# Performance work log

Hardware: AMD Instinct MI355X
Metric: run time of the kernel (lower is better)

The kernel has to match this reference:

```python
import jax, jax.numpy as jnp
import numpy as np

B, C, D, H = 2, 512, 512, 8
DH = D // H  # d_head = 64


def setup_inputs() -> dict:
    key = jax.random.key(0)
    ks = jax.random.split(key, 8)
    init = lambda k, shape: 0.02 * jax.random.normal(k, shape, dtype=jnp.float32)
    return {
        "x": jax.random.normal(ks[0], (B, C, D), dtype=jnp.float32),
        "Wq": init(ks[1], (D, D)), "bq": jnp.zeros((D,), jnp.float32),
        "Wk": init(ks[2], (D, D)), "bk": jnp.zeros((D,), jnp.float32),
        "Wv": init(ks[3], (D, D)), "bv": jnp.zeros((D,), jnp.float32),
        "W1": init(ks[4], (3 * DH, DH)), "b1": jnp.zeros((DH,), jnp.float32),
        "W2": init(ks[5], (DH, 1)), "b2": jnp.zeros((1,), jnp.float32),
        "Wo": init(ks[6], (D, D)), "bo": jnp.zeros((D,), jnp.float32),
    }


def reference(x, Wq, bq, Wk, bk, Wv, bv, W1, b1, W2, b2, Wo, bo):
    b, c, dm = x.shape
    # projections -> [B, H, C, d_head]
    q = (x @ Wq + bq).reshape(b, c, H, DH).transpose(0, 2, 1, 3)
    k = (x @ Wk + bk).reshape(b, c, H, DH).transpose(0, 2, 1, 3)
    v = (x @ Wv + bv).reshape(b, c, H, DH).transpose(0, 2, 1, 3)
    # split first MLP weight: [q || k || q*k] @ W1 = q@W1q + k@W1k + (q*k)@W1i
    W1q, W1k, W1i = W1[:DH], W1[DH:2 * DH], W1[2 * DH:]
    hq = jnp.einsum('bhid,de->bhie', q, W1q)   # [B,H,C,d]
    hk = jnp.einsum('bhjd,de->bhje', k, W1k)   # [B,H,C,d]
    hi = jnp.einsum('bhid,bhjd,de->bhije', q, k, W1i)  # [B,H,C,C,d] dominant intermediate
    h = hi + hq[:, :, :, None, :] + hk[:, :, None, :, :] + b1
    g = jax.nn.gelu(h, approximate=False)  # torch nn.GELU is exact erf form
    scores = (jnp.einsum('bhije,e->bhij', g, W2[:, 0]) + b2[0]) / (DH ** 0.5)
    attn = jax.nn.softmax(scores, axis=-1)  # dropout is identity in eval
    out = jnp.einsum('bhij,bhjd->bhid', attn, v)
    out = out.transpose(0, 2, 1, 3).reshape(b, c, dm)
    return out @ Wo + bo
```

## Files before the change

### kernel.cpp

```cpp
#include <hip/hip_runtime.h>
#include <hip/hip_bf16.h>
#include <math.h>

#define BB 2
#define CC 512
#define DD 512
#define HH 8
#define DH 64
#define TI 8

typedef __attribute__((ext_vector_type(8))) short short8;
typedef __attribute__((ext_vector_type(16))) float floatx16;
typedef __attribute__((ext_vector_type(2))) float float2v;
typedef unsigned short u16;

__device__ __forceinline__ float fast_rcp(float x) {
#if __has_builtin(__builtin_amdgcn_rcpf)
    return __builtin_amdgcn_rcpf(x);
#else
    return 1.0f / x;
#endif
}

__device__ __forceinline__ unsigned f2bf(float f) {
    unsigned u = __float_as_uint(f);
    u += 0x7FFF + ((u >> 16) & 1);
    return u >> 16;
}

__device__ __forceinline__ unsigned pk_bf16(float a, float b) {
    __hip_bfloat162 h2 = __float22bfloat162_rn(make_float2(a, b));
    unsigned r;
    __builtin_memcpy(&r, &h2, 4);
    return r;
}

__device__ __forceinline__ short8 mk_short8(unsigned u0, unsigned u1,
                                            unsigned u2, unsigned u3) {
    uint4 u = make_uint4(u0, u1, u2, u3);
    short8 r;
    __builtin_memcpy(&r, &u, 16);
    return r;
}

__device__ __forceinline__ float2v pkfma(float2v a, float2v b, float2v c) {
#if __has_builtin(__builtin_elementwise_fma)
    return __builtin_elementwise_fma(a, b, c);
#else
    float2v r; r[0] = fmaf(a[0], b[0], c[0]); r[1] = fmaf(a[1], b[1], c[1]);
    return r;
#endif
}

__device__ __forceinline__ void split_pack(const float* src, unsigned* hpk, unsigned* lpk) {
    #pragma unroll
    for (int p = 0; p < 4; ++p) {
        float a = src[2 * p], b = src[2 * p + 1];
        unsigned hp = pk_bf16(a, b);
        float la = a - __uint_as_float(hp << 16);
        float lb = b - __uint_as_float(hp & 0xffff0000u);
        hpk[p] = hp;
        lpk[p] = pk_bf16(la, lb);
    }
}

#define GC0 0.3989422804f
#define GC1 (-0.0664903801f)

__device__ __forceinline__ float2v gelu_dot2(float2v h, float2v w2, float2v p) {
    float2v s = h * h;
    float2v q = pkfma(s, float2v{GC1, GC1}, float2v{GC0, GC0});
    float2v t = s * q;
    float2v g = pkfma(h, float2v{0.5f, 0.5f}, t);
    return pkfma(g, w2, p);
}

__global__ __launch_bounds__(256) void prep(
    const float* __restrict__ Wq, const float* __restrict__ Wk,
    const float* __restrict__ Wv, const float* __restrict__ Wo,
    const float* __restrict__ W1, const float* __restrict__ b1,
    const float* __restrict__ bq,
    u16* __restrict__ wth, u16* __restrict__ wtl,
    u16* __restrict__ woh, u16* __restrict__ wol,
    float* __restrict__ b1p)
{
    __shared__ float SH[3 * 64 * 68];
    int j = blockIdx.x, t = threadIdx.x;
    if (j < 256) {
        int mat = j >> 6;
        const float* W = (mat == 0) ? Wq : (mat == 1) ? Wk : (mat == 2) ? Wv : Wo;
        u16* oh = (mat < 3) ? wth + (size_t)mat * 262144 : woh;
        u16* ol = (mat < 3) ? wtl + (size_t)mat * 262144 : wol;
        int tile = j & 63;
        int k0 = (tile >> 3) * 64, n0 = (tile & 7) * 64;
        float (*TT)[68] = (float(*)[68])SH;
        int r = t >> 4, c4 = (t & 15) * 4;
        #pragma unroll
        for (int rr = 0; rr < 4; ++rr) {
            int k = r + rr * 16;
            float4 v = *(const float4*)&W[(size_t)(k0 + k) * 512 + n0 + c4];
            TT[c4 + 0][k] = v.x; TT[c4 + 1][k] = v.y;
            TT[c4 + 2][k] = v.z; TT[c4 + 3][k] = v.w;
        }
        __syncthreads();
        int n = t >> 2, kc = (t & 3) * 16;
        #pragma unroll
        for (int g = 0; g < 2; ++g) {
            unsigned hpk[4], lpk[4];
            split_pack(&TT[n][kc + g * 8], hpk, lpk);
            *(uint4*)&oh[(size_t)(n0 + n) * 512 + k0 + kc + g * 8] =
                make_uint4(hpk[0], hpk[1], hpk[2], hpk[3]);
            *(uint4*)&ol[(size_t)(n0 + n) * 512 + k0 + kc + g * 8] =
                make_uint4(lpk[0], lpk[1], lpk[2], lpk[3]);
        }
    } else if (j < 320) {
        int jj = j - 256;
        int D0 = (jj >> 3) * 64, h = jj & 7;
        float (*WQ)[68]  = (float(*)[68])SH;
        float (*W1Q)[68] = (float(*)[68])(SH + 64 * 68);
        float (*OT)[68]  = (float(*)[68])(SH + 2 * 64 * 68);
        int r = t >> 4, c4 = (t & 15) * 4;
        #pragma unroll
        for (int rr = 0; rr < 4; ++rr) {
            int d = r + rr * 16;
            *(float4*)&WQ[d][c4]  = *(const float4*)&Wq[(size_t)(D0 + d) * 512 + h * 64 + c4];
            *(float4*)&W1Q[d][c4] = *(const float4*)&W1[(size_t)d * 64 + c4];
        }
        __syncthreads();
        int D = t & 63, ec = (t >> 6) * 16;
        float outv[16];
        #pragma unroll
        for (int i = 0; i < 16; ++i) outv[i] = 0.0f;
        for (int d4 = 0; d4 < 16; ++d4) {
            float4 wq4 = *(float4*)&WQ[D][d4 * 4];
            float wqa[4] = {wq4.x, wq4.y, wq4.z, wq4.w};
            #pragma unroll
            for (int dd = 0; dd < 4; ++dd) {
                float wv_ = wqa[dd];
                const float* wrow = &W1Q[d4 * 4 + dd][ec];
                #pragma unroll
                for (int i = 0; i < 16; ++i) outv[i] = fmaf(wv_, wrow[i], outv[i]);
            }
        }
        #pragma unroll
        for (int i = 0; i < 16; ++i) OT[ec + i][D] = outv[i];
        __syncthreads();
        int n = t >> 2, kc = (t & 3) * 16;
        u16* oh3 = wth + (size_t)3 * 262144;
        u16* ol3 = wtl + (size_t)3 * 262144;
        #pragma unroll
        for (int g = 0; g < 2; ++g) {
            unsigned hpk[4], lpk[4];
            split_pack(&OT[n][kc + g * 8], hpk, lpk);
            *(uint4*)&oh3[(size_t)(h * 64 + n) * 512 + D0 + kc + g * 8] =
                make_uint4(hpk[0], hpk[1], hpk[2], hpk[3]);
            *(uint4*)&ol3[(size_t)(h * 64 + n) * 512 + D0 + kc + g * 8] =
                make_uint4(lpk[0], lpk[1], lpk[2], lpk[3]);
        }
    } else {
        for (int n = t; n < 512; n += 256) {
            int h = n >> 6, e = n & 63;
            float s = b1[e];
            for (int d = 0; d < 64; ++d)
                s = fmaf(bq[h * 64 + d], W1[(size_t)d * 64 + e], s);
            b1p[n] = s;
        }
    }
}

__global__ __launch_bounds__(256) void gemm_qkv(
    const float* __restrict__ x,
    const u16* __restrict__ wth, const u16* __restrict__ wtl,
    const float* __restrict__ bq, const float* __restrict__ bk,
    const float* __restrict__ bv, const float* __restrict__ b1p,
    float* __restrict__ qw, float* __restrict__ kw, float* __restrict__ vw,
    float* __restrict__ hqc)
{
    __shared__ u16 Ah[64][64], Al[64][64], Bh[64][64], Bl[64][64];
    int t = threadIdx.x;
    int m0 = blockIdx.x * 64;
    int ny = blockIdx.y;
    int mat = ny >> 3, n0 = (ny & 7) * 64;
    const u16* WH = wth + (size_t)mat * 262144;
    const u16* WL = wtl + (size_t)mat * 262144;
    const float* bias = (mat == 0) ? bq : (mat == 1) ? bk : (mat == 2) ? bv : b1p;
    float* out = (mat == 0) ? qw : (mat == 1) ? kw : (mat == 2) ? vw : hqc;

    int lane = t & 63, w = t >> 6;
    int mrow = (w & 1) * 32, ncol = (w >> 1) * 32;
    int col = lane & 31, half = lane >> 5;
    int sr = t >> 2, skc = (t & 3) * 16;

    floatx16 acc = {0.0f,0.0f,0.0f,0.0f,0.0f,0.0f,0.0f,0.0f,
                    0.0f,0.0f,0.0f,0.0f,0.0f,0.0f,0.0f,0.0f};

    for (int k0 = 0; k0 < 512; k0 += 64) {
        float xa[16];
        const float* xr = &x[(size_t)(m0 + sr) * 512 + k0 + skc];
        *(float4*)&xa[0]  = *(const float4*)&xr[0];
        *(float4*)&xa[4]  = *(const float4*)&xr[4];
        *(float4*)&xa[8]  = *(const float4*)&xr[8];
        *(float4*)&xa[12] = *(const float4*)&xr[12];
        #pragma unroll
        for (int g = 0; g < 2; ++g) {
            unsigned hpk[4], lpk[4];
            split_pack(&xa[g * 8], hpk, lpk);
            int gg = (skc >> 3) + g;
            int sw = (gg ^ (sr & 7)) * 8;
            *(uint4*)&Ah[sr][sw] = make_uint4(hpk[0], hpk[1], hpk[2], hpk[3]);
            *(uint4*)&Al[sr][sw] = make_uint4(lpk[0], lpk[1], lpk[2], lpk[3]);
            *(uint4*)&Bh[sr][sw] = *(const uint4*)&WH[(size_t)(n0 + sr) * 512 + k0 + skc + g * 8];
            *(uint4*)&Bl[sr][sw] = *(const uint4*)&WL[(size_t)(n0 + sr) * 512 + k0 + skc + g * 8];
        }
        __syncthreads();
        int ar = mrow + col, br = ncol + col;
        #pragma unroll
        for (int kk = 0; kk < 4; ++kk) {
            int g8 = kk * 2 + half;
            short8 ah = *(short8*)&Ah[ar][(g8 ^ (ar & 7)) * 8];
            short8 al = *(short8*)&Al[ar][(g8 ^ (ar & 7)) * 8];
            short8 bh = *(short8*)&Bh[br][(g8 ^ (br & 7)) * 8];
            short8 bl = *(short8*)&Bl[br][(g8 ^ (br & 7)) * 8];
            acc = __builtin_amdgcn_mfma_f32_32x32x16_bf16(al, bh, acc, 0, 0, 0);
            acc = __builtin_amdgcn_mfma_f32_32x32x16_bf16(ah, bl, acc, 0, 0, 0);
            acc = __builtin_amdgcn_mfma_f32_32x32x16_bf16(ah, bh, acc, 0, 0, 0);
        }
        __syncthreads();
    }
    int h = n0 >> 6;
    int e = ncol + col;
    float bv_ = bias[n0 + e];
    #pragma unroll
    for (int reg = 0; reg < 16; ++reg) {
        int r = m0 + mrow + (reg & 3) + 8 * (reg >> 2) + 4 * half;
        int b = r >> 9, c = r & 511;
        out[((size_t)(b * HH + h) * CC + c) * DH + e] = acc[reg] + bv_;
    }
}

__global__ __launch_bounds__(256) void gemm_out(
    const float* __restrict__ ow,
    const u16* __restrict__ woh, const u16* __restrict__ wol,
    const float* __restrict__ bo, float* __restrict__ y)
{
    __shared__ u16 Ah[64][64], Al[64][64], Bh[64][64], Bl[64][64];
    int t = threadIdx.x;
    int m0 = blockIdx.x * 64, n0 = blockIdx.y * 64;
    int lane = t & 63, w = t >> 6;
    int mrow = (w & 1) * 32, ncol = (w >> 1) * 32;
    int col = lane & 31, half = lane >> 5;
    int sr = t >> 2, skc = (t & 3) * 16;

    floatx16 acc = {0.0f,0.0f,0.0f,0.0f,0.0f,0.0f,0.0f,0.0f,
                    0.0f,0.0f,0.0f,0.0f,0.0f,0.0f,0.0f,0.0f};
    int r = m0 + sr, b = r >> 9, c = r & 511;

    for (int k0 = 0; k0 < 512; k0 += 64) {
        int hh = k0 >> 6;
        float xa[16];
        const float* arow = &ow[((size_t)(b * HH + hh) * CC + c) * DH + skc];
        *(float4*)&xa[0]  = *(const float4*)&arow[0];
        *(float4*)&xa[4]  = *(const float4*)&arow[4];
        *(float4*)&xa[8]  = *(const float4*)&arow[8];
        *(float4*)&xa[12] = *(const float4*)&arow[12];
        #pragma unroll
        for (int g = 0; g < 2; ++g) {
            unsigned hpk[4], lpk[4];
            split_pack(&xa[g * 8], hpk, lpk);
            int gg = (skc >> 3) + g;
            int sw = (gg ^ (sr & 7)) * 8;
            *(uint4*)&Ah[sr][sw] = make_uint4(hpk[0], hpk[1], hpk[2], hpk[3]);
            *(uint4*)&Al[sr][sw] = make_uint4(lpk[0], lpk[1], lpk[2], lpk[3]);
            *(uint4*)&Bh[sr][sw] = *(const uint4*)&woh[(size_t)(n0 + sr) * 512 + k0 + skc + g * 8];
            *(uint4*)&Bl[sr][sw] = *(const uint4*)&wol[(size_t)(n0 + sr) * 512 + k0 + skc + g * 8];
        }
        __syncthreads();
        int ar = mrow + col, br = ncol + col;
        #pragma unroll
        for (int kk = 0; kk < 4; ++kk) {
            int g8 = kk * 2 + half;
            short8 ah = *(short8*)&Ah[ar][(g8 ^ (ar & 7)) * 8];
            short8 al = *(short8*)&Al[ar][(g8 ^ (ar & 7)) * 8];
            short8 bh = *(short8*)&Bh[br][(g8 ^ (br & 7)) * 8];
            short8 bl = *(short8*)&Bl[br][(g8 ^ (br & 7)) * 8];
            acc = __builtin_amdgcn_mfma_f32_32x32x16_bf16(al, bh, acc, 0, 0, 0);
            acc = __builtin_amdgcn_mfma_f32_32x32x16_bf16(ah, bl, acc, 0, 0, 0);
            acc = __builtin_amdgcn_mfma_f32_32x32x16_bf16(ah, bh, acc, 0, 0, 0);
        }
        __syncthreads();
    }
    float bv_ = bo[n0 + ncol + col];
    #pragma unroll
    for (int reg = 0; reg < 16; ++reg) {
        int r2 = m0 + mrow + (reg & 3) + 8 * (reg >> 2) + 4 * half;
        y[(size_t)r2 * 512 + n0 + ncol + col] = acc[reg] + bv_;
    }
}

__global__ __launch_bounds__(256, 2) void attn2(
    const float* qw, const float* __restrict__ kw,
    const float* __restrict__ vw, const float* __restrict__ hqc,
    const float* __restrict__ W1, const float* __restrict__ W2,
    const float* __restrict__ b2p,
    float* ow)
{
    __shared__ unsigned int w1pk[64][64];
    __shared__ u16 Alds[2][64][64];
    __shared__ u16 sc16[TI][512];

    int t = threadIdx.x;
    int lane = t & 63;
    int w = t >> 6;
    int h = lane >> 5;
    int col = lane & 31;

    int bh = blockIdx.x >> 6;
    int i0 = (blockIdx.x & 63) * TI;

    const float* qb  = qw  + ((size_t)bh * CC + i0) * DH;
    const float* hb  = hqc + ((size_t)bh * CC + i0) * DH;
    const float* kb  = kw  + (size_t)bh * CC * DH;
    const float* vb  = vw  + (size_t)bh * CC * DH;

    for (int idx = t; idx < 4096; idx += 256) {
        int d = idx >> 6, e = idx & 63;
        w1pk[d][e] = pk_bf16(W1[(128 + d) * 64 + e], W1[(64 + d) * 64 + e]);
    }

    short8 bfrag[4][4];
    for (int n = 0; n < 4; ++n) {
        int j = w * 128 + n * 32 + col;
        const float* kr = kb + (size_t)j * 64;
        #pragma unroll
        for (int kk = 0; kk < 4; ++kk) {
            int d = kk * 16 + h * 8;
            float4 k0 = *(const float4*)(kr + d);
            float4 k1 = *(const float4*)(kr + d + 4);
            bfrag[n][kk] = mk_short8(pk_bf16(k0.x, k0.y), pk_bf16(k0.z, k0.w),
                                     pk_bf16(k1.x, k1.y), pk_bf16(k1.z, k1.w));
        }
    }

    float2v w2p[2][8];
    #pragma unroll
    for (int m = 0; m < 2; ++m)
        #pragma unroll
        for (int gq = 0; gq < 8; ++gq) {
            int e = m * 32 + (gq >> 1) * 8 + h * 4 + (gq & 1) * 2;
            w2p[m][gq] = float2v{W2[e], W2[e + 1]};
        }

    __syncthreads();

    #define PRODUCE_A(ii, buf)                                                  \
    {                                                                           \
        int e = lane;                                                           \
        int sw = e & 7;                                                         \
        _Pragma("unroll")                                                       \
        for (int gg = 0; gg < 2; ++gg) {                                        \
            int g8 = w * 2 + gg;                                                \
            const float* qr = qb + (ii) * 64 + g8 * 8;                          \
            float4 q0 = *(const float4*)qr;                                     \
            float4 q1 = *(const float4*)(qr + 4);                               \
            float qv[8] = {q0.x, q0.y, q0.z, q0.w, q1.x, q1.y, q1.z, q1.w};     \
            unsigned int pk[4];                                                 \
            _Pragma("unroll")                                                   \
            for (int p2 = 0; p2 < 4; ++p2) {                                    \
                unsigned wp0 = w1pk[g8 * 8 + 2 * p2 + 0][e];                    \
                unsigned wp1 = w1pk[g8 * 8 + 2 * p2 + 1][e];                    \
                float w1i0 = __uint_as_float(wp0 << 16);                        \
                float w1k0 = __uint_as_float(wp0 & 0xffff0000u);                \
                float w1i1 = __uint_as_float(wp1 << 16);                        \
                float w1k1 = __uint_as_float(wp1 & 0xffff0000u);                \
                float a0 = fmaf(qv[2 * p2 + 0], w1i0, w1k0);                    \
                float a1 = fmaf(qv[2 * p2 + 1], w1i1, w1k1);                    \
                pk[p2] = pk_bf16(a0, a1);                                       \
            }                                                                   \
            *(uint4*)&Alds[buf][e][(g8 ^ sw) * 8] =                             \
                make_uint4(pk[0], pk[1], pk[2], pk[3]);                         \
        }                                                                       \
    }

    PRODUCE_A(0, 0);
    __syncthreads();

    for (int ii = 0; ii < TI; ++ii) {
        int cur = ii & 1;

        short8 afrag[2][4];
        #pragma unroll
        for (int m = 0; m < 2; ++m) {
            int e = m * 32 + col;
            int sw = e & 7;
            #pragma unroll
            for (int kk = 0; kk < 4; ++kk) {
                int g8 = kk * 2 + h;
                afrag[m][kk] = *(short8*)&Alds[cur][e][(g8 ^ sw) * 8];
            }
        }
        floatx16 csx[2];
        #pragma unroll
        for (int m = 0; m < 2; ++m)
            #pragma unroll
            for (int g = 0; g < 4; ++g) {
                float4 c4 = *(const float4*)&hb[ii * 64 + m * 32 + g * 8 + h * 4];
                csx[m][g * 4 + 0] = c4.x; csx[m][g * 4 + 1] = c4.y;
                csx[m][g * 4 + 2] = c4.z; csx[m][g * 4 + 3] = c4.w;
            }

        if (ii + 1 < TI) PRODUCE_A(ii + 1, cur ^ 1);

        #pragma unroll
        for (int n = 0; n < 4; ++n) {
            floatx16 acc[2];
            acc[0] = __builtin_amdgcn_mfma_f32_32x32x16_bf16(
                         afrag[0][0], bfrag[n][0], csx[0], 0, 0, 0);
            acc[1] = __builtin_amdgcn_mfma_f32_32x32x16_bf16(
                         afrag[1][0], bfrag[n][0], csx[1], 0, 0, 0);
            #pragma unroll
            for (int kk = 1; kk < 4; ++kk) {
                acc[0] = __builtin_amdgcn_mfma_f32_32x32x16_bf16(
                             afrag[0][kk], bfrag[n][kk], acc[0], 0, 0, 0);
                acc[1] = __builtin_amdgcn_mfma_f32_32x32x16_bf16(
                             afrag[1][kk], bfrag[n][kk], acc[1], 0, 0, 0);
            }
            float2v p2 = {0.0f, 0.0f};
            #pragma unroll
            for (int m = 0; m < 2; ++m)
                #pragma unroll
                for (int g = 0; g < 4; ++g)
                    #pragma unroll
                    for (int pr = 0; pr < 2; ++pr) {
                        float2v hvv = {acc[m][g * 4 + pr * 2],
                                       acc[m][g * 4 + pr * 2 + 1]};
                        p2 = gelu_dot2(hvv, w2p[m][g * 2 + pr], p2);
                    }
            float p = p2[0] + p2[1];
            p += __shfl_xor(p, 32);
            if (h == 0) sc16[ii][w * 128 + n * 32 + col] = (u16)pk_bf16(p, p);
        }
        __syncthreads();
    }
    #undef PRODUCE_A

    float* attn = (float*)w1pk;
    float b2v = b2p[0];
    for (int iirow = w; iirow < TI; iirow += 4) {
        float xv[8];
        float m = -1e30f;
        #pragma unroll
        for (int c = 0; c < 8; ++c) {
            float raw = __uint_as_float((unsigned)sc16[iirow][c * 64 + lane] << 16);
            xv[c] = (raw + b2v) * 0.125f;
            m = fmaxf(m, xv[c]);
        }
        #pragma unroll
        for (int o = 1; o < 64; o <<= 1) m = fmaxf(m, __shfl_xor(m, o));
        float s = 0.0f;
        #pragma unroll
        for (int c = 0; c < 8; ++c) { xv[c] = __expf(xv[c] - m); s += xv[c]; }
        #pragma unroll
        for (int o = 1; o < 64; o <<= 1) s += __shfl_xor(s, o);
        float r = fast_rcp(s);
        #pragma unroll
        for (int c = 0; c < 8; ++c) attn[iirow * 512 + c * 64 + lane] = xv[c] * r;
    }
    __syncthreads();

    {
        float* part = (float*)Alds;
        int e4 = (lane & 15) * 4;
        int ip = lane >> 4;
        int ia = 2 * ip, ib = ia + 1;
        float4 aA = {0.0f, 0.0f, 0.0f, 0.0f};
        float4 aB = {0.0f, 0.0f, 0.0f, 0.0f};
        int jbase = w * 128;
        int jrot = 8 * ip;
        #pragma unroll 4
        for (int jj = 0; jj < 128; ++jj) {
            int j = jbase + ((jj + jrot) & 127);
            float4 v4 = *(const float4*)&vb[(size_t)j * 64 + e4];
            float s0 = attn[ia * 512 + j], s1 = attn[ib * 512 + j];
            aA.x = fmaf(s0, v4.x, aA.x); aA.y = fmaf(s0, v4.y, aA.y);
            aA.z = fmaf(s0, v4.z, aA.z); aA.w = fmaf(s0, v4.w, aA.w);
            aB.x = fmaf(s1, v4.x, aB.x); aB.y = fmaf(s1, v4.y, aB.y);
            aB.z = fmaf(s1, v4.z, aB.z); aB.w = fmaf(s1, v4.w, aB.w);
        }
        *(float4*)&part[(w * 8 + ia) * 64 + e4] = aA;
        *(float4*)&part[(w * 8 + ib) * 64 + e4] = aB;
        __syncthreads();
        for (int idx = t; idx < 512; idx += 256) {
            int i = idx >> 6, e = idx & 63;
            float s = part[(0 + i) * 64 + e] + part[(8 + i) * 64 + e]
                    + part[(16 + i) * 64 + e] + part[(24 + i) * 64 + e];
            ow[((size_t)bh * CC + i0 + i) * DH + e] = s;
        }
    }
}

extern "C" void kernel_launch(void* const* d_in, const int* in_sizes, int n_in,
                              void* d_out, int out_size, void* d_ws, size_t ws_size,
                              hipStream_t stream)
{
    const float* x  = (const float*)d_in[0];
    const float* Wq = (const float*)d_in[1];
    const float* bq = (const float*)d_in[2];
    const float* Wk = (const float*)d_in[3];
    const float* bk = (const float*)d_in[4];
    const float* Wv = (const float*)d_in[5];
    const float* bv = (const float*)d_in[6];
    const float* W1 = (const float*)d_in[7];
    const float* b1 = (const float*)d_in[8];
    const float* W2 = (const float*)d_in[9];
    const float* b2 = (const float*)d_in[10];
    const float* Wo = (const float*)d_in[11];
    const float* bo = (const float*)d_in[12];
    float* y  = (float*)d_out;
    float* ws = (float*)d_ws;

    const size_t SEG = (size_t)BB * HH * CC * DH;
    float* qw  = ws;
    float* kw  = ws + SEG;
    float* vw  = ws + 2 * SEG;
    float* hqc = ws + 3 * SEG;
    u16*   wth = (u16*)(ws + 4 * SEG);
    u16*   wtl = (u16*)(ws + 5 * SEG);
    u16*   woh = (u16*)(ws + 6 * SEG);
    u16*   wol = (u16*)(ws + 6 * SEG + 131072);
    float* b1p = ws + 6 * SEG + 262144;
    float* ow  = qw;

    prep<<<dim3(321), 256, 0, stream>>>(Wq, Wk, Wv, Wo, W1, b1, bq,
                                        wth, wtl, woh, wol, b1p);
    gemm_qkv<<<dim3(16, 32), 256, 0, stream>>>(x, wth, wtl, bq, bk, bv, b1p,
                                               qw, kw, vw, hqc);
    attn2<<<dim3(1024), 256, 0, stream>>>(qw, kw, vw, hqc, W1, W2, b2, ow);
    gemm_out<<<dim3(16, 8), 256, 0, stream>>>(ow, woh, wol, bo, y);
}
```

Baseline: 200.2 us.

## Halve query rows per attention block and keep W1 slices in registers

Cuts rows per block from 8 to 4 and doubles the grid to 2048 blocks, for more parallelism and lower LDS use. The packed-bf16 W1 table in shared memory is replaced by per-thread fp32 register copies, which removes the LDS table, its unpacking and a barrier. The softmax and PV scratch buffers are remapped onto the remaining LDS arrays. The cost is that each block reloads all of K into bf16 fragments and V for half as many rows, so redundant global traffic doubles, and register pressure rises.

```diff
diff --git a/kernel.cpp b/kernel.cpp
--- a/kernel.cpp
+++ b/kernel.cpp
@@ -7,7 +7,7 @@
 #define DD 512
 #define HH 8
 #define DH 64
-#define TI 8
+#define TI 4
 
 typedef __attribute__((ext_vector_type(8))) short short8;
 typedef __attribute__((ext_vector_type(16))) float floatx16;
@@ -20,12 +20,6 @@
 #else
     return 1.0f / x;
 #endif
-}
-
-__device__ __forceinline__ unsigned f2bf(float f) {
-    unsigned u = __float_as_uint(f);
-    u += 0x7FFF + ((u >> 16) & 1);
-    return u >> 16;
 }
 
 __device__ __forceinline__ unsigned pk_bf16(float a, float b) {
@@ -304,7 +298,6 @@
     const float* __restrict__ b2p,
     float* ow)
 {
-    __shared__ unsigned int w1pk[64][64];
     __shared__ u16 Alds[2][64][64];
     __shared__ u16 sc16[TI][512];
 
@@ -314,17 +307,22 @@
     int h = lane >> 5;
     int col = lane & 31;
 
-    int bh = blockIdx.x >> 6;
-    int i0 = (blockIdx.x & 63) * TI;
+    int bh = blockIdx.x >> 7;
+    int i0 = (blockIdx.x & 127) * TI;
 
     const float* qb  = qw  + ((size_t)bh * CC + i0) * DH;
     const float* hb  = hqc + ((size_t)bh * CC + i0) * DH;
     const float* kb  = kw  + (size_t)bh * CC * DH;
     const float* vb  = vw  + (size_t)bh * CC * DH;
 
-    for (int idx = t; idx < 4096; idx += 256) {
-        int d = idx >> 6, e = idx & 63;
-        w1pk[d][e] = pk_bf16(W1[(128 + d) * 64 + e], W1[(64 + d) * 64 + e]);
+    float w1i_r[16], w1k_r[16];
+    {
+        int dbase = w * 16;
+        #pragma unroll
+        for (int dd = 0; dd < 16; ++dd) {
+            w1i_r[dd] = W1[(size_t)(128 + dbase + dd) * 64 + lane];
+            w1k_r[dd] = W1[(size_t)(64 + dbase + dd) * 64 + lane];
+        }
     }
 
     short8 bfrag[4][4];
@@ -349,8 +347,6 @@
             int e = m * 32 + (gq >> 1) * 8 + h * 4 + (gq & 1) * 2;
             w2p[m][gq] = float2v{W2[e], W2[e + 1]};
         }
-
-    __syncthreads();
 
     #define PRODUCE_A(ii, buf)                                                  \
     {                                                                           \
@@ -366,14 +362,10 @@
             unsigned int pk[4];                                                 \
             _Pragma("unroll")                                                   \
             for (int p2 = 0; p2 < 4; ++p2) {                                    \
-                unsigned wp0 = w1pk[g8 * 8 + 2 * p2 + 0][e];                    \
-                unsigned wp1 = w1pk[g8 * 8 + 2 * p2 + 1][e];                    \
-                float w1i0 = __uint_as_float(wp0 << 16);                        \
-                float w1k0 = __uint_as_float(wp0 & 0xffff0000u);                \
-                float w1i1 = __uint_as_float(wp1 << 16);                        \
-                float w1k1 = __uint_as_float(wp1 & 0xffff0000u);                \
-                float a0 = fmaf(qv[2 * p2 + 0], w1i0, w1k0);                    \
-                float a1 = fmaf(qv[2 * p2 + 1], w1i1, w1k1);                    \
+                float a0 = fmaf(qv[2 * p2 + 0], w1i_r[gg * 8 + 2 * p2 + 0],     \
+                                w1k_r[gg * 8 + 2 * p2 + 0]);                    \
+                float a1 = fmaf(qv[2 * p2 + 1], w1i_r[gg * 8 + 2 * p2 + 1],     \
+                                w1k_r[gg * 8 + 2 * p2 + 1]);                    \
                 pk[p2] = pk_bf16(a0, a1);                                       \
             }                                                                   \
             *(uint4*)&Alds[buf][e][(g8 ^ sw) * 8] =                             \
@@ -443,9 +435,10 @@
     }
     #undef PRODUCE_A
 
-    float* attn = (float*)w1pk;
+    float* attn = (float*)Alds;
     float b2v = b2p[0];
-    for (int iirow = w; iirow < TI; iirow += 4) {
+    {
+        int iirow = w;
         float xv[8];
         float m = -1e30f;
         #pragma unroll
@@ -468,31 +461,26 @@
     __syncthreads();
 
     {
-        float* part = (float*)Alds;
+        float* part = (float*)sc16;
         int e4 = (lane & 15) * 4;
         int ip = lane >> 4;
-        int ia = 2 * ip, ib = ia + 1;
         float4 aA = {0.0f, 0.0f, 0.0f, 0.0f};
-        float4 aB = {0.0f, 0.0f, 0.0f, 0.0f};
         int jbase = w * 128;
         int jrot = 8 * ip;
         #pragma unroll 4
         for (int jj = 0; jj < 128; ++jj) {
             int j = jbase + ((jj + jrot) & 127);
             float4 v4 = *(const float4*)&vb[(size_t)j * 64 + e4];
-            float s0 = attn[ia * 512 + j], s1 = attn[ib * 512 + j];
+            float s0 = attn[ip * 512 + j];
             aA.x = fmaf(s0, v4.x, aA.x); aA.y = fmaf(s0, v4.y, aA.y);
             aA.z = fmaf(s0, v4.z, aA.z); aA.w = fmaf(s0, v4.w, aA.w);
-            aB.x = fmaf(s1, v4.x, aB.x); aB.y = fmaf(s1, v4.y, aB.y);
-            aB.z = fmaf(s1, v4.z, aB.z); aB.w = fmaf(s1, v4.w, aB.w);
-        }
-        *(float4*)&part[(w * 8 + ia) * 64 + e4] = aA;
-        *(float4*)&part[(w * 8 + ib) * 64 + e4] = aB;
-        __syncthreads();
-        for (int idx = t; idx < 512; idx += 256) {
-            int i = idx >> 6, e = idx & 63;
-            float s = part[(0 + i) * 64 + e] + part[(8 + i) * 64 + e]
-                    + part[(16 + i) * 64 + e] + part[(24 + i) * 64 + e];
+        }
+        *(float4*)&part[(w * 4 + ip) * 64 + e4] = aA;
+        __syncthreads();
+        if (t < 256) {
+            int i = t >> 6, e = t & 63;
+            float s = part[(0 + i) * 64 + e] + part[(4 + i) * 64 + e]
+                    + part[(8 + i) * 64 + e] + part[(12 + i) * 64 + e];
             ow[((size_t)bh * CC + i0 + i) * DH + e] = s;
         }
     }
@@ -534,6 +522,6 @@
                                         wth, wtl, woh, wol, b1p);
     gemm_qkv<<<dim3(16, 32), 256, 0, stream>>>(x, wth, wtl, bq, bk, bv, b1p,
                                                qw, kw, vw, hqc);
-    attn2<<<dim3(1024), 256, 0, stream>>>(qw, kw, vw, hqc, W1, W2, b2, ow);
+    attn2<<<dim3(2048), 256, 0, stream>>>(qw, kw, vw, hqc, W1, W2, b2, ow);
     gemm_out<<<dim3(16, 8), 256, 0, stream>>>(ow, woh, wol, bo, y);
 }
```

After: 229.0 us. 1.14x slower.
